# Kernel tuning notes

Hardware: AMD Instinct MI355X
Metric: run time of the kernel (lower is better)

## Reference

```python
import jax, jax.numpy as jnp
import numpy as np

TN_LAYERS = 2
GCN_LAYERS = 2

def _gru(x, h0, Wih, Whh, bih, bhh):
    # x: (B,T,I), h0: (B,H) -> (B,T,H); torch nn.GRU gate math (r,z,n ordering)
    def step(h, xt):
        gi = xt @ Wih.T + bih
        gh = h @ Whh.T + bhh
        ir, iz, inn = jnp.split(gi, 3, axis=-1)
        hr, hz, hn = jnp.split(gh, 3, axis=-1)
        r = jax.nn.sigmoid(ir + hr)
        z = jax.nn.sigmoid(iz + hz)
        n = jnp.tanh(inn + r * hn)
        h_new = (1.0 - z) * n + z * h
        return h_new, h_new
    _, hs = jax.lax.scan(step, h0, jnp.swapaxes(x, 0, 1))
    return jnp.swapaxes(hs, 0, 1)

def _forward(x, x_mark, sp_emb, sp_W1, sp_b1, sp_W2, sp_b2, t_emb, t_Wih, t_Whh, t_bih, t_bhh,
             gcn_W, gcn_b, fr_W1, fr_b1, fr_W2, fr_b2, tr_Wih, tr_Whh, tr_bih, tr_bhh, out_W, out_b):
    B, T, N = x.shape
    L = sp_b1.shape[0]
    elu = jax.nn.elu
    # --- SpatialEncoder: (B,N,T) ++ static embed -> Linear,ELU,Linear -> (B,N,L)
    xs = jnp.swapaxes(x, 1, 2)
    xs = jnp.concatenate([xs, jnp.broadcast_to(sp_emb, (B,) + sp_emb.shape)], axis=-1)
    Xs = elu(xs @ sp_W1 + sp_b1) @ sp_W2 + sp_b2
    # --- TemporalEncoder: concat(x, x_mark, static time embed) -> GRU -> (B,T,L)
    xt = jnp.concatenate([x, x_mark, jnp.broadcast_to(t_emb, (B,) + t_emb.shape)], axis=-1)
    Xt = _gru(xt, jnp.zeros((B, L), x.dtype), t_Wih, t_Whh, t_bih, t_bhh)
    X = jnp.concatenate([Xs, Xt], axis=1)  # (B, N+T, L)
    # --- TN modules: dynamic adjacency tanh(relu(X X^T)) + weighted message passing.
    # The torch code extracts per-batch sparse edge lists from batch_adj and does
    # gather-weight-scatter over them; zero-weight edges contribute nothing, so this
    # equals dense weighted aggregation A @ X per batch.
    for ti in range(TN_LAYERS):
        A = jnp.tanh(jax.nn.relu(jnp.einsum('bnf,bmf->bnm', X, X)))  # (B,N+T,N+T)
        for li in range(GCN_LAYERS):
            X = elu(jnp.einsum('bnm,bmd->bnd', A, X) @ gcn_W[ti, li] + gcn_b[ti, li])
    # --- Rebuild branches
    Xs2, Xt2 = X[:, :N, :], X[:, N:, :]
    rs = elu(Xs2 @ fr_W1 + fr_b1) @ fr_W2 + fr_b2  # feature_rebuild: (B,N,T)
    rt = _gru(Xt2, jnp.zeros((B, N), x.dtype), tr_Wih, tr_Whh, tr_bih, tr_bhh)  # time_rebuild: (B,T,N)
    combined = rs + jnp.swapaxes(rt, 1, 2)  # (B,N,T)
    return combined @ out_W + out_b  # (B, N, out_seq_len)

def setup_inputs():
    key = jax.random.key(0)
    B, T, N, Dt, L, E = 8, 96, 2000, 4, 32, 32
    ks = iter(jax.random.split(key, 32))
    nrm = lambda shape, s: jax.random.normal(next(ks), shape, jnp.float32) * s
    return {
        'x': nrm((B, T, N), 1.0),
        'x_mark': nrm((B, T, Dt), 1.0),
        'sp_emb': nrm((N, E), 0.1),
        'sp_W1': nrm((T + E, L), (T + E) ** -0.5), 'sp_b1': jnp.zeros((L,), jnp.float32),
        'sp_W2': nrm((L, L), L ** -0.5), 'sp_b2': jnp.zeros((L,), jnp.float32),
        't_emb': nrm((T, E), 0.1),
        't_Wih': nrm((3 * L, N + Dt + E), (N + Dt + E) ** -0.5),
        't_Whh': nrm((3 * L, L), L ** -0.5),
        't_bih': jnp.zeros((3 * L,), jnp.float32), 't_bhh': jnp.zeros((3 * L,), jnp.float32),
        'gcn_W': nrm((TN_LAYERS, GCN_LAYERS, L, L), 3e-3),  # small scale: dense aggregation sums ~N+T terms
        'gcn_b': jnp.zeros((TN_LAYERS, GCN_LAYERS, L), jnp.float32),
        'fr_W1': nrm((L, T), L ** -0.5), 'fr_b1': jnp.zeros((T,), jnp.float32),
        'fr_W2': nrm((T, T), T ** -0.5), 'fr_b2': jnp.zeros((T,), jnp.float32),
        'tr_Wih': nrm((3 * N, L), L ** -0.5), 'tr_Whh': nrm((3 * N, N), N ** -0.5),
        'tr_bih': jnp.zeros((3 * N,), jnp.float32), 'tr_bhh': jnp.zeros((3 * N,), jnp.float32),
        'out_W': nrm((T, 1), T ** -0.5), 'out_b': jnp.zeros((1,), jnp.float32),
    }

def reference(x, x_mark, sp_emb, sp_W1, sp_b1, sp_W2, sp_b2, t_emb, t_Wih, t_Whh, t_bih, t_bhh,
              gcn_W, gcn_b, fr_W1, fr_b1, fr_W2, fr_b2, tr_Wih, tr_Whh, tr_bih, tr_bhh, out_W, out_b):
    return _forward(x, x_mark, sp_emb, sp_W1, sp_b1, sp_W2, sp_b2, t_emb, t_Wih, t_Whh, t_bih, t_bhh,
                    gcn_W, gcn_b, fr_W1, fr_b1, fr_W2, fr_b2, tr_Wih, tr_Whh, tr_bih, tr_bhh, out_W, out_b)
```

## Files before the change

kernel.cpp:

```cpp
#include <hip/hip_runtime.h>

typedef _Float16 half8 __attribute__((ext_vector_type(8)));
typedef float f32x4 __attribute__((ext_vector_type(4)));

#define NBLK 125
#define BAR_INTS (NBLK * 32)

__global__ __launch_bounds__(256) void k_spatial(
    const float* __restrict__ x, const float* __restrict__ sp_emb,
    const float* __restrict__ W1, const float* __restrict__ b1,
    const float* __restrict__ W2, const float* __restrict__ b2,
    _Float16* __restrict__ X, int* __restrict__ bar, unsigned char* __restrict__ hA) {
  __shared__ float W1s[128 * 32];
  __shared__ float W2s[32 * 32];
  __shared__ float b1s[32], b2s[32];
  int tid = threadIdx.x;
  int gidx = blockIdx.x * 256 + tid;
  for (int i = gidx; i < BAR_INTS; i += 63 * 256) bar[i] = 0;
  for (int i = gidx; i < 4000; i += 63 * 256) ((unsigned int*)hA)[i] = 0u;
  for (int i = tid; i < 128 * 32; i += 256) W1s[i] = W1[i];
  for (int i = tid; i < 32 * 32; i += 256) W2s[i] = W2[i];
  if (tid < 32) { b1s[tid] = b1[tid]; b2s[tid] = b2[tid]; }
  __syncthreads();
  if (gidx >= 8 * 2000) return;
  int b = gidx / 2000, n = gidx % 2000;
  float h1[32];
#pragma unroll
  for (int l = 0; l < 32; l++) h1[l] = b1s[l];
  for (int k = 0; k < 96; k++) {
    float xv = x[((size_t)b * 96 + k) * 2000 + n];
#pragma unroll
    for (int l = 0; l < 32; l++) h1[l] = fmaf(xv, W1s[k * 32 + l], h1[l]);
  }
  for (int e4 = 0; e4 < 8; e4++) {
    float4 ev = *reinterpret_cast<const float4*>(&sp_emb[(size_t)n * 32 + e4 * 4]);
    float evs[4] = {ev.x, ev.y, ev.z, ev.w};
#pragma unroll
    for (int q = 0; q < 4; q++) {
      int e = e4 * 4 + q;
#pragma unroll
      for (int l = 0; l < 32; l++) h1[l] = fmaf(evs[q], W1s[(96 + e) * 32 + l], h1[l]);
    }
  }
  float out[32];
#pragma unroll
  for (int j = 0; j < 32; j++) out[j] = b2s[j];
  for (int l = 0; l < 32; l++) {
    float a = h1[l] > 0.0f ? h1[l] : (__expf(h1[l]) - 1.0f);
#pragma unroll
    for (int j = 0; j < 32; j++) out[j] = fmaf(a, W2s[l * 32 + j], out[j]);
  }
  _Float16* dst = X + ((size_t)b * 2096 + n) * 32;
#pragma unroll
  for (int j8 = 0; j8 < 4; j8++) {
    half8 v;
#pragma unroll
    for (int q = 0; q < 8; q++) v[q] = (_Float16)out[j8 * 8 + q];
    *reinterpret_cast<half8*>(dst + j8 * 8) = v;
  }
}

__global__ __launch_bounds__(256) void k_tgi(
    const float* __restrict__ x, const float* __restrict__ x_mark,
    const float* __restrict__ t_emb, const float* __restrict__ Wih,
    const float* __restrict__ bih, float* __restrict__ gi) {
  __shared__ float xs[8][2036];
  int tid = threadIdx.x;
  int row0 = blockIdx.x * 8;
  for (int rr = 0; rr < 8; rr++) {
    int row = row0 + rr;
    int b = row / 96, t = row % 96;
    for (int k = tid; k < 2036; k += 256) {
      float v;
      if (k < 2000) v = x[((size_t)b * 96 + t) * 2000 + k];
      else if (k < 2004) v = x_mark[((size_t)b * 96 + t) * 4 + (k - 2000)];
      else v = t_emb[(size_t)t * 32 + (k - 2004)];
      xs[rr][k] = v;
    }
  }
  __syncthreads();
  for (int oi = tid; oi < 8 * 96; oi += 256) {
    int rr = oi & 7, g = oi >> 3;
    const float* w = Wih + (size_t)g * 2036;
    float acc = bih[g];
    for (int k = 0; k < 2036; k += 4) {
      float4 wv = *reinterpret_cast<const float4*>(w + k);
      acc = fmaf(xs[rr][k + 0], wv.x, acc);
      acc = fmaf(xs[rr][k + 1], wv.y, acc);
      acc = fmaf(xs[rr][k + 2], wv.z, acc);
      acc = fmaf(xs[rr][k + 3], wv.w, acc);
    }
    gi[(size_t)(row0 + rr) * 96 + g] = acc;
  }
}

__global__ __launch_bounds__(768) void k_tgru(
    const float* __restrict__ gi, const float* __restrict__ Whh,
    const float* __restrict__ bhh, _Float16* __restrict__ X) {
  __shared__ float Whs[96][33];
  __shared__ float hs[8][33];
  __shared__ float ga[3][8][33];
  int tid = threadIdx.x;
  for (int i = tid; i < 96 * 32; i += 768) Whs[i >> 5][i & 31] = Whh[i];
  if (tid < 256) hs[tid >> 5][tid & 31] = 0.0f;
  int g = tid >> 8, j = (tid >> 3) & 31, b = tid & 7;
  int row = g * 32 + j;
  float bb0 = 0.f, bb1 = 0.f, bb2 = 0.f;
  if (tid < 256) {
    int jj = tid & 31;
    bb0 = bhh[jj]; bb1 = bhh[32 + jj]; bb2 = bhh[64 + jj];
  }
  __syncthreads();
  for (int t = 0; t < 96; t++) {
    float acc = 0.0f;
#pragma unroll
    for (int k = 0; k < 32; k++) acc = fmaf(hs[b][k], Whs[row][k], acc);
    ga[g][b][j] = acc;
    __syncthreads();
    if (tid < 256) {
      int bb = tid >> 5, jj = tid & 31;
      const float* gp = gi + ((size_t)bb * 96 + t) * 96;
      float gr = ga[0][bb][jj] + bb0;
      float gz = ga[1][bb][jj] + bb1;
      float gn = ga[2][bb][jj] + bb2;
      float r = 1.0f / (1.0f + __expf(-(gp[jj] + gr)));
      float z = 1.0f / (1.0f + __expf(-(gp[32 + jj] + gz)));
      float n = tanhf(gp[64 + jj] + r * gn);
      float hn = (1.0f - z) * n + z * hs[bb][jj];
      hs[bb][jj] = hn;
      X[((size_t)bb * 2096 + 2000 + t) * 32 + jj] = (_Float16)hn;
    }
    __syncthreads();
  }
}

__global__ __launch_bounds__(256) void k_gnn(
    const _Float16* __restrict__ Xa, const _Float16* __restrict__ Xin,
    _Float16* __restrict__ Xout, const float* __restrict__ W,
    const float* __restrict__ bias) {
  __shared__ _Float16 XaR[32][40];
  __shared__ _Float16 Xm[2][64][40];
  __shared__ _Float16 Xq[2][64][40];
  __shared__ _Float16 At[32][72];
  __shared__ float Pm[32][36];
  __shared__ float Ws[32][36];
  __shared__ float bs[32];
  int tid = threadIdx.x;
  int l = tid & 63, w = tid >> 6;
  int b = blockIdx.y;
  int r0 = blockIdx.x * 32;
  const _Float16* Xab = Xa + (size_t)b * 2096 * 32;
  const _Float16* Xib = Xin + (size_t)b * 2096 * 32;
  half8 hz = {(_Float16)0, (_Float16)0, (_Float16)0, (_Float16)0,
              (_Float16)0, (_Float16)0, (_Float16)0, (_Float16)0};

  for (int i = tid; i < 1024; i += 256) Ws[i >> 5][i & 31] = W[i];
  if (tid < 32) bs[tid] = bias[tid];
  if (tid < 128) {
    int r = tid >> 2, k = (tid & 3) * 8;
    half8 v = (r0 + r < 2096)
                  ? *reinterpret_cast<const half8*>(Xab + (size_t)(r0 + r) * 32 + k)
                  : hz;
    *reinterpret_cast<half8*>(&XaR[r][k]) = v;
  }
  int sr = tid >> 2, sk = (tid & 3) * 8;
  {
    *reinterpret_cast<half8*>(&Xm[0][sr][sk]) =
        *reinterpret_cast<const half8*>(Xab + (size_t)sr * 32 + sk);
    *reinterpret_cast<half8*>(&Xq[0][sr][sk]) =
        *reinterpret_cast<const half8*>(Xib + (size_t)sr * 32 + sk);
  }
  __syncthreads();

  int lr = l & 15, lk = (l >> 4) * 8, lq = (l >> 4) * 4;
  int smt = w >> 1, snt2 = w & 1;
  int pmt = w >> 1, pnt = w & 1;
  half8 afrag = *reinterpret_cast<const half8*>(&XaR[smt * 16 + lr][lk]);
  f32x4 pacc = {0.f, 0.f, 0.f, 0.f};

  for (int tt = 0; tt < 33; tt++) {
    int cur = tt & 1, nb = cur ^ 1;
    half8 vm = hz, vq = hz;
    bool hv = (tt + 1 < 33);
    if (hv) {
      int gm = (tt + 1) * 64 + sr;
      if (gm < 2096) {
        vm = *reinterpret_cast<const half8*>(Xab + (size_t)gm * 32 + sk);
        vq = *reinterpret_cast<const half8*>(Xib + (size_t)gm * 32 + sk);
      }
    }
#pragma unroll
    for (int n16 = 0; n16 < 2; n16++) {
      int c0 = snt2 * 32 + n16 * 16;
      half8 bfrag = *reinterpret_cast<const half8*>(&Xm[cur][c0 + lr][lk]);
      f32x4 s4 = __builtin_amdgcn_mfma_f32_16x16x32_f16(
          afrag, bfrag, (f32x4){0.f, 0.f, 0.f, 0.f}, 0, 0, 0);
#pragma unroll
      for (int j = 0; j < 4; j++) {
        float e = __expf(-2.0f * fmaxf(s4[j], 0.0f));
        At[smt * 16 + lq + j][c0 + lr] = (_Float16)((1.0f - e) / (1.0f + e));
      }
    }
    __syncthreads();
#pragma unroll
    for (int kc = 0; kc < 2; kc++) {
      half8 af = *reinterpret_cast<const half8*>(&At[pmt * 16 + lr][kc * 32 + lk]);
      half8 bf;
      int kb = kc * 32 + lk;
      int nn = pnt * 16 + lr;
#pragma unroll
      for (int e = 0; e < 8; e++) bf[e] = Xq[cur][kb + e][nn];
      pacc = __builtin_amdgcn_mfma_f32_16x16x32_f16(af, bf, pacc, 0, 0, 0);
    }
    if (hv) {
      *reinterpret_cast<half8*>(&Xm[nb][sr][sk]) = vm;
      *reinterpret_cast<half8*>(&Xq[nb][sr][sk]) = vq;
    }
    __syncthreads();
  }

#pragma unroll
  for (int j = 0; j < 4; j++) Pm[pmt * 16 + lq + j][pnt * 16 + lr] = pacc[j];
  __syncthreads();
  int r = tid & 31, fgr = tid >> 5;
  int f0 = fgr * 4;
  float o[4];
#pragma unroll
  for (int j = 0; j < 4; j++) o[j] = bs[f0 + j];
#pragma unroll
  for (int k = 0; k < 32; k++) {
    float mv = Pm[r][k];
    float4 wv = *reinterpret_cast<const float4*>(&Ws[k][f0]);
    o[0] = fmaf(mv, wv.x, o[0]);
    o[1] = fmaf(mv, wv.y, o[1]);
    o[2] = fmaf(mv, wv.z, o[2]);
    o[3] = fmaf(mv, wv.w, o[3]);
  }
  int grr = r0 + r;
  if (grr < 2096) {
    _Float16* dst = Xout + ((size_t)b * 2096 + grr) * 32 + f0;
#pragma unroll
    for (int j = 0; j < 4; j++) {
      float v = o[j];
      dst[j] = (_Float16)(v > 0.0f ? v : (__expf(v) - 1.0f));
    }
  }
}

__global__ __launch_bounds__(1024) void k_trgru(
    const _Float16* __restrict__ X, const float* __restrict__ wih,
    const float* __restrict__ bih, float* __restrict__ gi,
    const float* __restrict__ whh, const float* __restrict__ bhh,
    unsigned char* __restrict__ hA, unsigned char* __restrict__ hB,
    float* __restrict__ rt, int* __restrict__ seq,
    const float* __restrict__ frW1, const float* __restrict__ frb1,
    const float* __restrict__ frW2, const float* __restrict__ frb2,
    float* __restrict__ rs) {
  __shared__ __align__(16) unsigned char SM[139264];
  int tid = threadIdx.x;
  int blk = blockIdx.x;

  if (blk >= NBLK) {
    float* W1s = (float*)(SM);
    float* W2s = (float*)(SM + 12288);
    float* b1s = (float*)(SM + 50688);
    float* b2s = (float*)(SM + 51072);
    float* Xt  = (float*)(SM + 51456);
    float* Hl  = (float*)(SM + 55680);
    for (int i = tid; i < 32 * 96; i += 1024) W1s[i] = frW1[i];
    for (int i = tid; i < 96 * 96; i += 1024) W2s[(i / 96) * 100 + (i % 96)] = frW2[i];
    if (tid < 96) { b1s[tid] = frb1[tid]; b2s[tid] = frb2[tid]; }
    __syncthreads();
    for (int ti = blk - NBLK; ti < 504; ti += NBLK) {
      int b = ti / 63, n0 = (ti % 63) * 32;
      {
        int r = tid >> 5, k = tid & 31;
        Xt[r * 33 + k] =
            (n0 + r < 2000) ? (float)X[((size_t)b * 2096 + n0 + r) * 32 + k] : 0.0f;
      }
      __syncthreads();
#pragma unroll
      for (int q = 0; q < 3; q++) {
        int idx = q * 1024 + tid;
        int r = idx / 96, c = idx % 96;
        float a = b1s[c];
#pragma unroll 8
        for (int k = 0; k < 32; k++) a = fmaf(Xt[r * 33 + k], W1s[k * 96 + c], a);
        Hl[r * 100 + c] = a > 0.0f ? a : (__expf(a) - 1.0f);
      }
      __syncthreads();
#pragma unroll
      for (int q = 0; q < 3; q++) {
        int idx = q * 1024 + tid;
        int r = idx / 96, c = idx % 96;
        float o = b2s[c];
#pragma unroll 8
        for (int k = 0; k < 96; k++) o = fmaf(Hl[r * 100 + k], W2s[k * 100 + c], o);
        if (n0 + r < 2000) rs[((size_t)b * 2000 + n0 + r) * 96 + c] = o;
      }
      __syncthreads();
    }
    return;
  }

  unsigned char* wf = SM;
  unsigned char* hf = SM + 98304;
  float* pt = (float*)(SM + 114688);
  int l = tid & 63, w = tid >> 6;

  for (int i = tid; i < 12288; i += 1024) ((unsigned long long*)wf)[i] = 0ull;
  for (int i = tid; i < 2048; i += 1024) ((unsigned long long*)hf)[i] = 0ull;

  if (tid < 768) {
    int t = tid >> 3, b = tid & 7;
    float xr[32];
    const _Float16* xp = X + ((size_t)b * 2096 + 2000 + t) * 32;
#pragma unroll
    for (int k = 0; k < 32; k++) xr[k] = (float)xp[k];
    float* gp = gi + ((size_t)b * 96 + t) * 6000;
    for (int g = 0; g < 3; g++) {
#pragma unroll
      for (int j = 0; j < 16; j++) {
        int row = g * 2000 + blk * 16 + j;
        const float* wr = wih + (size_t)row * 32;
        float a = bih[row];
#pragma unroll 8
        for (int k = 0; k < 32; k++) a = fmaf(xr[k], wr[k], a);
        gp[row] = a;
      }
    }
  }
  __syncthreads();

  for (int i = tid; i < 3 * 64 * 64; i += 1024) {
    int g = i >> 12;
    int c = (i >> 6) & 63;
    int l2 = i & 63;
    int j = l2 & 15;
    int k0 = c * 32 + ((l2 >> 4) << 3);
    if (k0 <= 1992) {
      const float* src = whh + ((size_t)(g * 2000 + blk * 16 + j)) * 2000 + k0;
      float4 v0 = *reinterpret_cast<const float4*>(src);
      float4 v1 = *reinterpret_cast<const float4*>(src + 4);
      unsigned int lo = __builtin_amdgcn_cvt_pk_fp8_f32(v0.x, v0.y, 0, false);
      lo = __builtin_amdgcn_cvt_pk_fp8_f32(v0.z, v0.w, lo, true);
      unsigned int hi = __builtin_amdgcn_cvt_pk_fp8_f32(v1.x, v1.y, 0, false);
      hi = __builtin_amdgcn_cvt_pk_fp8_f32(v1.z, v1.w, hi, true);
      unsigned long long q = ((unsigned long long)hi << 32) | (unsigned long long)lo;
      *reinterpret_cast<unsigned long long*>(wf + (size_t)g * 32768 + c * 512 + l2 * 8) = q;
    }
  }

  int cj = tid >> 3, cb = tid & 7;
  int jg = blk * 16 + cj;
  float hold = 0.0f, bR = 0.f, bZ = 0.f, bN = 0.f;
  if (tid < 128) {
    bR = bhh[jg]; bZ = bhh[2000 + jg]; bN = bhh[4000 + jg];
  }
  int bslot = ((l >> 4) * 8 + (l & 7)) * 8;
  __syncthreads();

  for (int t = 0; t < 96; t++) {
    const unsigned char* hc = (t & 1) ? hB : hA;
    unsigned char* hn = (t & 1) ? hA : hB;
    float gir = 0.f, giz = 0.f, gin = 0.f;
    if (tid < 128) {
      const float* gp = gi + ((size_t)cb * 96 + t) * 6000;
      gir = gp[jg]; giz = gp[2000 + jg]; gin = gp[4000 + jg];
    }
    for (int i = tid; i < 2048; i += 1024) {
      int c = i >> 5, s = i & 31;
      int b = s & 7;
      int k0 = c * 32 + ((s >> 3) << 3);
      if (k0 < 2000) {
        unsigned long long v =
            *reinterpret_cast<const unsigned long long*>(hc + b * 2000 + k0);
        *reinterpret_cast<unsigned long long*>(hf + c * 256 + s * 8) = v;
      }
    }
    __syncthreads();
    f32x4 a0 = {0.f, 0.f, 0.f, 0.f}, a1 = {0.f, 0.f, 0.f, 0.f}, a2 = {0.f, 0.f, 0.f, 0.f};
#pragma unroll
    for (int i = 0; i < 4; i++) {
      int c = w * 4 + i;
      long long bv = *reinterpret_cast<const long long*>(hf + c * 256 + bslot);
      long long w0 = *reinterpret_cast<const long long*>(wf + 0 * 32768 + c * 512 + l * 8);
      long long w1 = *reinterpret_cast<const long long*>(wf + 1 * 32768 + c * 512 + l * 8);
      long long w2 = *reinterpret_cast<const long long*>(wf + 2 * 32768 + c * 512 + l * 8);
      a0 = __builtin_amdgcn_mfma_f32_16x16x32_fp8_fp8(w0, bv, a0, 0, 0, 0);
      a1 = __builtin_amdgcn_mfma_f32_16x16x32_fp8_fp8(w1, bv, a1, 0, 0, 0);
      a2 = __builtin_amdgcn_mfma_f32_16x16x32_fp8_fp8(w2, bv, a2, 0, 0, 0);
    }
    {
      int bcol = l & 15;
      if (bcol < 8) {
        int lb = l >> 4;
        *reinterpret_cast<f32x4*>(pt + w * 384 + 0 * 128 + lb * 32 + bcol * 4) = a0;
        *reinterpret_cast<f32x4*>(pt + w * 384 + 1 * 128 + lb * 32 + bcol * 4) = a1;
        *reinterpret_cast<f32x4*>(pt + w * 384 + 2 * 128 + lb * 32 + bcol * 4) = a2;
      }
    }
    __syncthreads();
    if (tid < 128) {
      float s[3];
#pragma unroll
      for (int g = 0; g < 3; g++) {
        int base = g * 128 + (cj >> 2) * 32 + cb * 4 + (cj & 3);
        float acc = 0.f;
#pragma unroll
        for (int w2 = 0; w2 < 16; w2++) acc += pt[w2 * 384 + base];
        s[g] = acc;
      }
      float r_ = 1.0f / (1.0f + __expf(-(gir + s[0] + bR)));
      float z_ = 1.0f / (1.0f + __expf(-(giz + s[1] + bZ)));
      float n_ = tanhf(gin + r_ * (s[2] + bN));
      hold = (1.0f - z_) * n_ + z_ * hold;
      {
        unsigned int p = __builtin_amdgcn_cvt_pk_fp8_f32(hold, 0.0f, 0, false);
        __hip_atomic_store(hn + cb * 2000 + jg, (unsigned char)(p & 0xFF),
                           __ATOMIC_RELAXED, __HIP_MEMORY_SCOPE_AGENT);
      }
      rt[((size_t)cb * 96 + t) * 2000 + jg] = hold;
    }
    __syncthreads();
    if (tid == 0) {
      __hip_atomic_store(&seq[blk * 32], t + 1, __ATOMIC_RELAXED,
                         __HIP_MEMORY_SCOPE_AGENT);
    }
    if ((tid >> 6) == 2) {
      int lane = tid & 63;
      const int* s1 = &seq[lane * 32];
      const int* s2 = &seq[((lane + 64) < NBLK ? (lane + 64) : lane) * 32];
      while (true) {
        int v1 = __hip_atomic_load(s1, __ATOMIC_RELAXED, __HIP_MEMORY_SCOPE_AGENT);
        int v2 = __hip_atomic_load(s2, __ATOMIC_RELAXED, __HIP_MEMORY_SCOPE_AGENT);
        if (__all(v1 > t && v2 > t)) break;
        __builtin_amdgcn_s_sleep(1);
      }
      if (lane == 0) {
        (void)__hip_atomic_load(s1, __ATOMIC_ACQUIRE, __HIP_MEMORY_SCOPE_AGENT);
      }
    }
    __syncthreads();
  }
}

__global__ __launch_bounds__(256) void k_final(
    const float* __restrict__ rs, const float* __restrict__ rt,
    const float* __restrict__ outW, const float* __restrict__ outb,
    float* __restrict__ out) {
  __shared__ float w[96];
  __shared__ float ob;
  int tid = threadIdx.x;
  if (tid < 96) w[tid] = outW[tid];
  if (tid == 0) ob = outb[0];
  __syncthreads();
  int gidx = blockIdx.x * 256 + tid;
  if (gidx >= 16000) return;
  int b = gidx / 2000, n = gidx % 2000;
  const float* rsp = rs + (size_t)gidx * 96;
  float acc = ob;
  for (int t4 = 0; t4 < 24; t4++) {
    float4 rv = *reinterpret_cast<const float4*>(rsp + t4 * 4);
    int t = t4 * 4;
    acc = fmaf(rv.x + rt[((size_t)b * 96 + t + 0) * 2000 + n], w[t + 0], acc);
    acc = fmaf(rv.y + rt[((size_t)b * 96 + t + 1) * 2000 + n], w[t + 1], acc);
    acc = fmaf(rv.z + rt[((size_t)b * 96 + t + 2) * 2000 + n], w[t + 2], acc);
    acc = fmaf(rv.w + rt[((size_t)b * 96 + t + 3) * 2000 + n], w[t + 3], acc);
  }
  out[gidx] = acc;
}

extern "C" void kernel_launch(void* const* d_in, const int* in_sizes, int n_in,
                              void* d_out, int out_size, void* d_ws, size_t ws_size,
                              hipStream_t stream) {
  const float* x      = (const float*)d_in[0];
  const float* x_mark = (const float*)d_in[1];
  const float* sp_emb = (const float*)d_in[2];
  const float* sp_W1  = (const float*)d_in[3];
  const float* sp_b1  = (const float*)d_in[4];
  const float* sp_W2  = (const float*)d_in[5];
  const float* sp_b2  = (const float*)d_in[6];
  const float* t_emb  = (const float*)d_in[7];
  const float* t_Wih  = (const float*)d_in[8];
  const float* t_Whh  = (const float*)d_in[9];
  const float* t_bih  = (const float*)d_in[10];
  const float* t_bhh  = (const float*)d_in[11];
  const float* gcn_W  = (const float*)d_in[12];
  const float* gcn_b  = (const float*)d_in[13];
  const float* fr_W1  = (const float*)d_in[14];
  const float* fr_b1  = (const float*)d_in[15];
  const float* fr_W2  = (const float*)d_in[16];
  const float* fr_b2  = (const float*)d_in[17];
  const float* tr_Wih = (const float*)d_in[18];
  const float* tr_Whh = (const float*)d_in[19];
  const float* tr_bih = (const float*)d_in[20];
  const float* tr_bhh = (const float*)d_in[21];
  const float* out_W  = (const float*)d_in[22];
  const float* out_b  = (const float*)d_in[23];
  (void)in_sizes; (void)n_in; (void)out_size; (void)ws_size;

  float* ws = (float*)d_ws;
  float* X0   = ws;
  float* X1   = X0 + 536576;
  float* X2   = X1 + 536576;
  float* tgi  = X2 + 536576;
  float* trgi = tgi + 73728;
  float* hsl  = trgi + 4608000;
  float* rt   = hsl + 16000;
  float* rs   = rt + 1536000;
  float* barf = rs + 1536000;

  _Float16* X0h = (_Float16*)X0;
  _Float16* X1h = (_Float16*)X1;
  _Float16* X2h = (_Float16*)X2;
  unsigned char* hA = (unsigned char*)hsl;
  unsigned char* hB = hA + 16000;
  int* seq = (int*)barf;

  k_spatial<<<63, 256, 0, stream>>>(x, sp_emb, sp_W1, sp_b1, sp_W2, sp_b2, X0h, seq, hA);
  k_tgi<<<96, 256, 0, stream>>>(x, x_mark, t_emb, t_Wih, t_bih, tgi);
  k_tgru<<<1, 768, 0, stream>>>(tgi, t_Whh, t_bhh, X0h);

  dim3 gg(66, 8);
  k_gnn<<<gg, 256, 0, stream>>>(X0h, X0h, X1h, gcn_W + 0 * 1024, gcn_b + 0 * 32);
  k_gnn<<<gg, 256, 0, stream>>>(X0h, X1h, X2h, gcn_W + 1 * 1024, gcn_b + 1 * 32);
  k_gnn<<<gg, 256, 0, stream>>>(X2h, X2h, X0h, gcn_W + 2 * 1024, gcn_b + 2 * 32);
  k_gnn<<<gg, 256, 0, stream>>>(X2h, X0h, X1h, gcn_W + 3 * 1024, gcn_b + 3 * 32);

  {
    const _Float16* a0 = X1h;
    const float* a1 = tr_Wih;
    const float* a2 = tr_bih;
    float* a3 = trgi;
    const float* a4 = tr_Whh;
    const float* a5 = tr_bhh;
    unsigned char* a6 = hA;
    unsigned char* a7 = hB;
    float* a8 = rt;
    int* a9 = seq;
    const float* a10 = fr_W1;
    const float* a11 = fr_b1;
    const float* a12 = fr_W2;
    const float* a13 = fr_b2;
    float* a14 = rs;
    void* cargs[] = {&a0, &a1, &a2, &a3, &a4, &a5, &a6, &a7,
                     &a8, &a9, &a10, &a11, &a12, &a13, &a14};
    hipLaunchCooperativeKernel((const void*)k_trgru, dim3(250), dim3(1024), cargs, 0, stream);
  }

  k_final<<<63, 256, 0, stream>>>(rs, rt, out_W, out_b, (float*)d_out);
}
```

Measured before the change: 1.001 ms.

## Merge prologue kernels, fuse final projection into cooperative GRU, transpose GNN operand

```diff
diff --git a/kernel.cpp b/kernel.cpp
--- a/kernel.cpp
+++ b/kernel.cpp
@@ -4,93 +4,96 @@
 typedef float f32x4 __attribute__((ext_vector_type(4)));
 
 #define NBLK 125
-#define BAR_INTS (NBLK * 32)
-
-__global__ __launch_bounds__(256) void k_spatial(
-    const float* __restrict__ x, const float* __restrict__ sp_emb,
-    const float* __restrict__ W1, const float* __restrict__ b1,
-    const float* __restrict__ W2, const float* __restrict__ b2,
-    _Float16* __restrict__ X, int* __restrict__ bar, unsigned char* __restrict__ hA) {
-  __shared__ float W1s[128 * 32];
-  __shared__ float W2s[32 * 32];
-  __shared__ float b1s[32], b2s[32];
+#define TOTBLK 250
+#define BAR_INTS (TOTBLK * 32)
+
+__global__ __launch_bounds__(256) void k_pre(
+    const float* __restrict__ x, const float* __restrict__ x_mark,
+    const float* __restrict__ sp_emb,
+    const float* __restrict__ spW1, const float* __restrict__ spb1,
+    const float* __restrict__ spW2, const float* __restrict__ spb2,
+    const float* __restrict__ t_emb, const float* __restrict__ tWih,
+    const float* __restrict__ tbih,
+    _Float16* __restrict__ X, float* __restrict__ gi,
+    int* __restrict__ seq, unsigned char* __restrict__ hA) {
+  __shared__ __align__(16) unsigned char PSM[65152];
   int tid = threadIdx.x;
-  int gidx = blockIdx.x * 256 + tid;
-  for (int i = gidx; i < BAR_INTS; i += 63 * 256) bar[i] = 0;
-  for (int i = gidx; i < 4000; i += 63 * 256) ((unsigned int*)hA)[i] = 0u;
-  for (int i = tid; i < 128 * 32; i += 256) W1s[i] = W1[i];
-  for (int i = tid; i < 32 * 32; i += 256) W2s[i] = W2[i];
-  if (tid < 32) { b1s[tid] = b1[tid]; b2s[tid] = b2[tid]; }
-  __syncthreads();
-  if (gidx >= 8 * 2000) return;
-  int b = gidx / 2000, n = gidx % 2000;
-  float h1[32];
-#pragma unroll
-  for (int l = 0; l < 32; l++) h1[l] = b1s[l];
-  for (int k = 0; k < 96; k++) {
-    float xv = x[((size_t)b * 96 + k) * 2000 + n];
-#pragma unroll
-    for (int l = 0; l < 32; l++) h1[l] = fmaf(xv, W1s[k * 32 + l], h1[l]);
-  }
-  for (int e4 = 0; e4 < 8; e4++) {
-    float4 ev = *reinterpret_cast<const float4*>(&sp_emb[(size_t)n * 32 + e4 * 4]);
-    float evs[4] = {ev.x, ev.y, ev.z, ev.w};
-#pragma unroll
-    for (int q = 0; q < 4; q++) {
-      int e = e4 * 4 + q;
-#pragma unroll
-      for (int l = 0; l < 32; l++) h1[l] = fmaf(evs[q], W1s[(96 + e) * 32 + l], h1[l]);
-    }
-  }
-  float out[32];
-#pragma unroll
-  for (int j = 0; j < 32; j++) out[j] = b2s[j];
-  for (int l = 0; l < 32; l++) {
-    float a = h1[l] > 0.0f ? h1[l] : (__expf(h1[l]) - 1.0f);
-#pragma unroll
-    for (int j = 0; j < 32; j++) out[j] = fmaf(a, W2s[l * 32 + j], out[j]);
-  }
-  _Float16* dst = X + ((size_t)b * 2096 + n) * 32;
-#pragma unroll
-  for (int j8 = 0; j8 < 4; j8++) {
-    half8 v;
-#pragma unroll
-    for (int q = 0; q < 8; q++) v[q] = (_Float16)out[j8 * 8 + q];
-    *reinterpret_cast<half8*>(dst + j8 * 8) = v;
-  }
-}
-
-__global__ __launch_bounds__(256) void k_tgi(
-    const float* __restrict__ x, const float* __restrict__ x_mark,
-    const float* __restrict__ t_emb, const float* __restrict__ Wih,
-    const float* __restrict__ bih, float* __restrict__ gi) {
-  __shared__ float xs[8][2036];
-  int tid = threadIdx.x;
-  int row0 = blockIdx.x * 8;
-  for (int rr = 0; rr < 8; rr++) {
-    int row = row0 + rr;
-    int b = row / 96, t = row % 96;
-    for (int k = tid; k < 2036; k += 256) {
-      float v;
-      if (k < 2000) v = x[((size_t)b * 96 + t) * 2000 + k];
-      else if (k < 2004) v = x_mark[((size_t)b * 96 + t) * 4 + (k - 2000)];
-      else v = t_emb[(size_t)t * 32 + (k - 2004)];
-      xs[rr][k] = v;
-    }
-  }
-  __syncthreads();
-  for (int oi = tid; oi < 8 * 96; oi += 256) {
-    int rr = oi & 7, g = oi >> 3;
-    const float* w = Wih + (size_t)g * 2036;
-    float acc = bih[g];
-    for (int k = 0; k < 2036; k += 4) {
-      float4 wv = *reinterpret_cast<const float4*>(w + k);
-      acc = fmaf(xs[rr][k + 0], wv.x, acc);
-      acc = fmaf(xs[rr][k + 1], wv.y, acc);
-      acc = fmaf(xs[rr][k + 2], wv.z, acc);
-      acc = fmaf(xs[rr][k + 3], wv.w, acc);
-    }
-    gi[(size_t)(row0 + rr) * 96 + g] = acc;
+  if (blockIdx.x < 63) {
+    float* W1s = (float*)PSM;
+    float* W2s = (float*)(PSM + 16384);
+    float* b1s = (float*)(PSM + 20480);
+    float* b2s = (float*)(PSM + 20608);
+    int gidx = blockIdx.x * 256 + tid;
+    for (int i = gidx; i < BAR_INTS; i += 63 * 256) seq[i] = 0;
+    for (int i = gidx; i < 4000; i += 63 * 256) ((unsigned int*)hA)[i] = 0u;
+    for (int i = tid; i < 128 * 32; i += 256) W1s[i] = spW1[i];
+    for (int i = tid; i < 32 * 32; i += 256) W2s[i] = spW2[i];
+    if (tid < 32) { b1s[tid] = spb1[tid]; b2s[tid] = spb2[tid]; }
+    __syncthreads();
+    if (gidx >= 8 * 2000) return;
+    int b = gidx / 2000, n = gidx % 2000;
+    float h1[32];
+#pragma unroll
+    for (int l = 0; l < 32; l++) h1[l] = b1s[l];
+    for (int k = 0; k < 96; k++) {
+      float xv = x[((size_t)b * 96 + k) * 2000 + n];
+#pragma unroll
+      for (int l = 0; l < 32; l++) h1[l] = fmaf(xv, W1s[k * 32 + l], h1[l]);
+    }
+    for (int e4 = 0; e4 < 8; e4++) {
+      float4 ev = *reinterpret_cast<const float4*>(&sp_emb[(size_t)n * 32 + e4 * 4]);
+      float evs[4] = {ev.x, ev.y, ev.z, ev.w};
+#pragma unroll
+      for (int q = 0; q < 4; q++) {
+        int e = e4 * 4 + q;
+#pragma unroll
+        for (int l = 0; l < 32; l++) h1[l] = fmaf(evs[q], W1s[(96 + e) * 32 + l], h1[l]);
+      }
+    }
+    float out[32];
+#pragma unroll
+    for (int j = 0; j < 32; j++) out[j] = b2s[j];
+    for (int l = 0; l < 32; l++) {
+      float a = h1[l] > 0.0f ? h1[l] : (__expf(h1[l]) - 1.0f);
+#pragma unroll
+      for (int j = 0; j < 32; j++) out[j] = fmaf(a, W2s[l * 32 + j], out[j]);
+    }
+    _Float16* dst = X + ((size_t)b * 2096 + n) * 32;
+#pragma unroll
+    for (int j8 = 0; j8 < 4; j8++) {
+      half8 v;
+#pragma unroll
+      for (int q = 0; q < 8; q++) v[q] = (_Float16)out[j8 * 8 + q];
+      *reinterpret_cast<half8*>(dst + j8 * 8) = v;
+    }
+  } else {
+    float (*xs)[2036] = (float(*)[2036])PSM;
+    int row0 = (blockIdx.x - 63) * 8;
+    for (int rr = 0; rr < 8; rr++) {
+      int row = row0 + rr;
+      int b = row / 96, t = row % 96;
+      for (int k = tid; k < 2036; k += 256) {
+        float v;
+        if (k < 2000) v = x[((size_t)b * 96 + t) * 2000 + k];
+        else if (k < 2004) v = x_mark[((size_t)b * 96 + t) * 4 + (k - 2000)];
+        else v = t_emb[(size_t)t * 32 + (k - 2004)];
+        xs[rr][k] = v;
+      }
+    }
+    __syncthreads();
+    for (int oi = tid; oi < 8 * 96; oi += 256) {
+      int rr = oi & 7, g = oi >> 3;
+      const float* w = tWih + (size_t)g * 2036;
+      float acc = tbih[g];
+      for (int k = 0; k < 2036; k += 4) {
+        float4 wv = *reinterpret_cast<const float4*>(w + k);
+        acc = fmaf(xs[rr][k + 0], wv.x, acc);
+        acc = fmaf(xs[rr][k + 1], wv.y, acc);
+        acc = fmaf(xs[rr][k + 2], wv.z, acc);
+        acc = fmaf(xs[rr][k + 3], wv.w, acc);
+      }
+      gi[(size_t)(row0 + rr) * 96 + g] = acc;
+    }
   }
 }
 
@@ -140,7 +143,7 @@
     const float* __restrict__ bias) {
   __shared__ _Float16 XaR[32][40];
   __shared__ _Float16 Xm[2][64][40];
-  __shared__ _Float16 Xq[2][64][40];
+  __shared__ _Float16 XqT[2][32][72];
   __shared__ _Float16 At[32][72];
   __shared__ float Pm[32][36];
   __shared__ float Ws[32][36];
@@ -167,8 +170,9 @@
   {
     *reinterpret_cast<half8*>(&Xm[0][sr][sk]) =
         *reinterpret_cast<const half8*>(Xab + (size_t)sr * 32 + sk);
-    *reinterpret_cast<half8*>(&Xq[0][sr][sk]) =
-        *reinterpret_cast<const half8*>(Xib + (size_t)sr * 32 + sk);
+    half8 vq = *reinterpret_cast<const half8*>(Xib + (size_t)sr * 32 + sk);
+#pragma unroll
+    for (int e = 0; e < 8; e++) XqT[0][sk + e][sr] = vq[e];
   }
   __syncthreads();
 
@@ -202,19 +206,19 @@
       }
     }
     __syncthreads();
-#pragma unroll
-    for (int kc = 0; kc < 2; kc++) {
-      half8 af = *reinterpret_cast<const half8*>(&At[pmt * 16 + lr][kc * 32 + lk]);
-      half8 bf;
-      int kb = kc * 32 + lk;
+    {
       int nn = pnt * 16 + lr;
 #pragma unroll
-      for (int e = 0; e < 8; e++) bf[e] = Xq[cur][kb + e][nn];
-      pacc = __builtin_amdgcn_mfma_f32_16x16x32_f16(af, bf, pacc, 0, 0, 0);
+      for (int kc = 0; kc < 2; kc++) {
+        half8 af = *reinterpret_cast<const half8*>(&At[pmt * 16 + lr][kc * 32 + lk]);
+        half8 bf = *reinterpret_cast<const half8*>(&XqT[cur][nn][kc * 32 + lk]);
+        pacc = __builtin_amdgcn_mfma_f32_16x16x32_f16(af, bf, pacc, 0, 0, 0);
+      }
     }
     if (hv) {
       *reinterpret_cast<half8*>(&Xm[nb][sr][sk]) = vm;
-      *reinterpret_cast<half8*>(&Xq[nb][sr][sk]) = vq;
+#pragma unroll
+      for (int e = 0; e < 8; e++) XqT[nb][sk + e][sr] = vq[e];
     }
     __syncthreads();
   }
@@ -255,8 +259,9 @@
     float* __restrict__ rt, int* __restrict__ seq,
     const float* __restrict__ frW1, const float* __restrict__ frb1,
     const float* __restrict__ frW2, const float* __restrict__ frb2,
-    float* __restrict__ rs) {
-  __shared__ __align__(16) unsigned char SM[139264];
+    float* __restrict__ rs, const float* __restrict__ outW,
+    const float* __restrict__ outb, float* __restrict__ out) {
+  __shared__ __align__(16) unsigned char SM[122880];
   int tid = threadIdx.x;
   int blk = blockIdx.x;
 
@@ -296,179 +301,190 @@
         float o = b2s[c];
 #pragma unroll 8
         for (int k = 0; k < 96; k++) o = fmaf(Hl[r * 100 + k], W2s[k * 100 + c], o);
-        if (n0 + r < 2000) rs[((size_t)b * 2000 + n0 + r) * 96 + c] = o;
+        if (n0 + r < 2000) {
+          __hip_atomic_store(&rs[((size_t)b * 2000 + n0 + r) * 96 + c], o,
+                             __ATOMIC_RELAXED, __HIP_MEMORY_SCOPE_AGENT);
+        }
       }
       __syncthreads();
     }
-    return;
-  }
-
-  unsigned char* wf = SM;
-  unsigned char* hf = SM + 98304;
-  float* pt = (float*)(SM + 114688);
-  int l = tid & 63, w = tid >> 6;
-
-  for (int i = tid; i < 12288; i += 1024) ((unsigned long long*)wf)[i] = 0ull;
-  for (int i = tid; i < 2048; i += 1024) ((unsigned long long*)hf)[i] = 0ull;
-
-  if (tid < 768) {
-    int t = tid >> 3, b = tid & 7;
-    float xr[32];
-    const _Float16* xp = X + ((size_t)b * 2096 + 2000 + t) * 32;
-#pragma unroll
-    for (int k = 0; k < 32; k++) xr[k] = (float)xp[k];
-    float* gp = gi + ((size_t)b * 96 + t) * 6000;
-    for (int g = 0; g < 3; g++) {
-#pragma unroll
-      for (int j = 0; j < 16; j++) {
-        int row = g * 2000 + blk * 16 + j;
-        const float* wr = wih + (size_t)row * 32;
-        float a = bih[row];
+    if (tid == 0) {
+      __hip_atomic_store(&seq[blk * 32], 96, __ATOMIC_RELAXED,
+                         __HIP_MEMORY_SCOPE_AGENT);
+    }
+  } else {
+    unsigned char* wf = SM;
+    float* pt = (float*)(SM + 98304);
+    int l = tid & 63, w = tid >> 6;
+
+    for (int i = tid; i < 12288; i += 1024) ((unsigned long long*)wf)[i] = 0ull;
+
+    if (tid < 768) {
+      int t = tid >> 3, b = tid & 7;
+      float xr[32];
+      const _Float16* xp = X + ((size_t)b * 2096 + 2000 + t) * 32;
+#pragma unroll
+      for (int k = 0; k < 32; k++) xr[k] = (float)xp[k];
+      float* gp = gi + ((size_t)b * 96 + t) * 6000;
+      for (int g = 0; g < 3; g++) {
+#pragma unroll
+        for (int j = 0; j < 16; j++) {
+          int row = g * 2000 + blk * 16 + j;
+          const float* wr = wih + (size_t)row * 32;
+          float a = bih[row];
 #pragma unroll 8
-        for (int k = 0; k < 32; k++) a = fmaf(xr[k], wr[k], a);
-        gp[row] = a;
-      }
-    }
-  }
-  __syncthreads();
-
-  for (int i = tid; i < 3 * 64 * 64; i += 1024) {
-    int g = i >> 12;
-    int c = (i >> 6) & 63;
-    int l2 = i & 63;
-    int j = l2 & 15;
-    int k0 = c * 32 + ((l2 >> 4) << 3);
-    if (k0 <= 1992) {
-      const float* src = whh + ((size_t)(g * 2000 + blk * 16 + j)) * 2000 + k0;
-      float4 v0 = *reinterpret_cast<const float4*>(src);
-      float4 v1 = *reinterpret_cast<const float4*>(src + 4);
-      unsigned int lo = __builtin_amdgcn_cvt_pk_fp8_f32(v0.x, v0.y, 0, false);
-      lo = __builtin_amdgcn_cvt_pk_fp8_f32(v0.z, v0.w, lo, true);
-      unsigned int hi = __builtin_amdgcn_cvt_pk_fp8_f32(v1.x, v1.y, 0, false);
-      hi = __builtin_amdgcn_cvt_pk_fp8_f32(v1.z, v1.w, hi, true);
-      unsigned long long q = ((unsigned long long)hi << 32) | (unsigned long long)lo;
-      *reinterpret_cast<unsigned long long*>(wf + (size_t)g * 32768 + c * 512 + l2 * 8) = q;
-    }
-  }
-
-  int cj = tid >> 3, cb = tid & 7;
-  int jg = blk * 16 + cj;
-  float hold = 0.0f, bR = 0.f, bZ = 0.f, bN = 0.f;
-  if (tid < 128) {
-    bR = bhh[jg]; bZ = bhh[2000 + jg]; bN = bhh[4000 + jg];
-  }
-  int bslot = ((l >> 4) * 8 + (l & 7)) * 8;
-  __syncthreads();
-
-  for (int t = 0; t < 96; t++) {
-    const unsigned char* hc = (t & 1) ? hB : hA;
-    unsigned char* hn = (t & 1) ? hA : hB;
-    float gir = 0.f, giz = 0.f, gin = 0.f;
+          for (int k = 0; k < 32; k++) a = fmaf(xr[k], wr[k], a);
+          gp[row] = a;
+        }
+      }
+    }
+
+    for (int i = tid; i < 3 * 64 * 64; i += 1024) {
+      int g = i >> 12;
+      int c = (i >> 6) & 63;
+      int l2 = i & 63;
+      int j = l2 & 15;
+      int k0 = c * 32 + ((l2 >> 4) << 3);
+      if (k0 <= 1992) {
+        const float* src = whh + ((size_t)(g * 2000 + blk * 16 + j)) * 2000 + k0;
+        float4 v0 = *reinterpret_cast<const float4*>(src);
+        float4 v1 = *reinterpret_cast<const float4*>(src + 4);
+        unsigned int lo = __builtin_amdgcn_cvt_pk_fp8_f32(v0.x, v0.y, 0, false);
+        lo = __builtin_amdgcn_cvt_pk_fp8_f32(v0.z, v0.w, lo, true);
+        unsigned int hi = __builtin_amdgcn_cvt_pk_fp8_f32(v1.x, v1.y, 0, false);
+        hi = __builtin_amdgcn_cvt_pk_fp8_f32(v1.z, v1.w, hi, true);
+        unsigned long long q = ((unsigned long long)hi << 32) | (unsigned long long)lo;
+        *reinterpret_cast<unsigned long long*>(wf + (size_t)g * 32768 + c * 512 + l2 * 8) = q;
+      }
+    }
+
+    int cj = tid >> 3, cb = tid & 7;
+    int jg = blk * 16 + cj;
+    float hold = 0.0f, bR = 0.f, bZ = 0.f, bN = 0.f;
     if (tid < 128) {
-      const float* gp = gi + ((size_t)cb * 96 + t) * 6000;
-      gir = gp[jg]; giz = gp[2000 + jg]; gin = gp[4000 + jg];
-    }
-    for (int i = tid; i < 2048; i += 1024) {
-      int c = i >> 5, s = i & 31;
-      int b = s & 7;
-      int k0 = c * 32 + ((s >> 3) << 3);
-      if (k0 < 2000) {
-        unsigned long long v =
-            *reinterpret_cast<const unsigned long long*>(hc + b * 2000 + k0);
-        *reinterpret_cast<unsigned long long*>(hf + c * 256 + s * 8) = v;
-      }
-    }
-    __syncthreads();
-    f32x4 a0 = {0.f, 0.f, 0.f, 0.f}, a1 = {0.f, 0.f, 0.f, 0.f}, a2 = {0.f, 0.f, 0.f, 0.f};
-#pragma unroll
-    for (int i = 0; i < 4; i++) {
-      int c = w * 4 + i;
-      long long bv = *reinterpret_cast<const long long*>(hf + c * 256 + bslot);
-      long long w0 = *reinterpret_cast<const long long*>(wf + 0 * 32768 + c * 512 + l * 8);
-      long long w1 = *reinterpret_cast<const long long*>(wf + 1 * 32768 + c * 512 + l * 8);
-      long long w2 = *reinterpret_cast<const long long*>(wf + 2 * 32768 + c * 512 + l * 8);
-      a0 = __builtin_amdgcn_mfma_f32_16x16x32_fp8_fp8(w0, bv, a0, 0, 0, 0);
-      a1 = __builtin_amdgcn_mfma_f32_16x16x32_fp8_fp8(w1, bv, a1, 0, 0, 0);
-      a2 = __builtin_amdgcn_mfma_f32_16x16x32_fp8_fp8(w2, bv, a2, 0, 0, 0);
-    }
-    {
-      int bcol = l & 15;
-      if (bcol < 8) {
-        int lb = l >> 4;
-        *reinterpret_cast<f32x4*>(pt + w * 384 + 0 * 128 + lb * 32 + bcol * 4) = a0;
-        *reinterpret_cast<f32x4*>(pt + w * 384 + 1 * 128 + lb * 32 + bcol * 4) = a1;
-        *reinterpret_cast<f32x4*>(pt + w * 384 + 2 * 128 + lb * 32 + bcol * 4) = a2;
-      }
-    }
-    __syncthreads();
-    if (tid < 128) {
-      float s[3];
-#pragma unroll
-      for (int g = 0; g < 3; g++) {
-        int base = g * 128 + (cj >> 2) * 32 + cb * 4 + (cj & 3);
-        float acc = 0.f;
-#pragma unroll
-        for (int w2 = 0; w2 < 16; w2++) acc += pt[w2 * 384 + base];
-        s[g] = acc;
-      }
-      float r_ = 1.0f / (1.0f + __expf(-(gir + s[0] + bR)));
-      float z_ = 1.0f / (1.0f + __expf(-(giz + s[1] + bZ)));
-      float n_ = tanhf(gin + r_ * (s[2] + bN));
-      hold = (1.0f - z_) * n_ + z_ * hold;
+      bR = bhh[jg]; bZ = bhh[2000 + jg]; bN = bhh[4000 + jg];
+    }
+    int bb = l & 7, kblk = (l >> 4) * 8;
+    __syncthreads();
+
+    for (int t = 0; t < 96; t++) {
+      const unsigned char* hc = (t & 1) ? hB : hA;
+      unsigned char* hn = (t & 1) ? hA : hB;
+      float gir = 0.f, giz = 0.f, gin = 0.f;
+      if (tid < 128) {
+        const float* gp = gi + ((size_t)cb * 96 + t) * 6000;
+        gir = gp[jg]; giz = gp[2000 + jg]; gin = gp[4000 + jg];
+      }
+      f32x4 a0 = {0.f, 0.f, 0.f, 0.f}, a1 = {0.f, 0.f, 0.f, 0.f}, a2 = {0.f, 0.f, 0.f, 0.f};
+#pragma unroll
+      for (int i = 0; i < 4; i++) {
+        int c = w * 4 + i;
+        int k0 = c * 32 + kblk;
+        long long bv = 0;
+        if (k0 <= 1992)
+          bv = *reinterpret_cast<const long long*>(hc + bb * 2000 + k0);
+        long long w0 = *reinterpret_cast<const long long*>(wf + 0 * 32768 + c * 512 + l * 8);
+        long long w1 = *reinterpret_cast<const long long*>(wf + 1 * 32768 + c * 512 + l * 8);
+        long long w2 = *reinterpret_cast<const long long*>(wf + 2 * 32768 + c * 512 + l * 8);
+        a0 = __builtin_amdgcn_mfma_f32_16x16x32_fp8_fp8(w0, bv, a0, 0, 0, 0);
+        a1 = __builtin_amdgcn_mfma_f32_16x16x32_fp8_fp8(w1, bv, a1, 0, 0, 0);
+        a2 = __builtin_amdgcn_mfma_f32_16x16x32_fp8_fp8(w2, bv, a2, 0, 0, 0);
+      }
       {
-        unsigned int p = __builtin_amdgcn_cvt_pk_fp8_f32(hold, 0.0f, 0, false);
-        __hip_atomic_store(hn + cb * 2000 + jg, (unsigned char)(p & 0xFF),
+        int bcol = l & 15;
+        if (bcol < 8) {
+          int lb = l >> 4;
+          *reinterpret_cast<f32x4*>(pt + w * 384 + 0 * 128 + lb * 32 + bcol * 4) = a0;
+          *reinterpret_cast<f32x4*>(pt + w * 384 + 1 * 128 + lb * 32 + bcol * 4) = a1;
+          *reinterpret_cast<f32x4*>(pt + w * 384 + 2 * 128 + lb * 32 + bcol * 4) = a2;
+        }
+      }
+      __syncthreads();
+      if (tid < 128) {
+        float s[3];
+#pragma unroll
+        for (int g = 0; g < 3; g++) {
+          int base = g * 128 + (cj >> 2) * 32 + cb * 4 + (cj & 3);
+          float acc = 0.f;
+#pragma unroll
+          for (int w2 = 0; w2 < 16; w2++) acc += pt[w2 * 384 + base];
+          s[g] = acc;
+        }
+        float r_ = 1.0f / (1.0f + __expf(-(gir + s[0] + bR)));
+        float z_ = 1.0f / (1.0f + __expf(-(giz + s[1] + bZ)));
+        float n_ = tanhf(gin + r_ * (s[2] + bN));
+        hold = (1.0f - z_) * n_ + z_ * hold;
+        {
+          unsigned int p = __builtin_amdgcn_cvt_pk_fp8_f32(hold, 0.0f, 0, false);
+          __hip_atomic_store(hn + cb * 2000 + jg, (unsigned char)(p & 0xFF),
+                             __ATOMIC_RELAXED, __HIP_MEMORY_SCOPE_AGENT);
+        }
+        __hip_atomic_store(&rt[((size_t)cb * 96 + t) * 2000 + jg], hold,
                            __ATOMIC_RELAXED, __HIP_MEMORY_SCOPE_AGENT);
       }
-      rt[((size_t)cb * 96 + t) * 2000 + jg] = hold;
-    }
-    __syncthreads();
-    if (tid == 0) {
-      __hip_atomic_store(&seq[blk * 32], t + 1, __ATOMIC_RELAXED,
-                         __HIP_MEMORY_SCOPE_AGENT);
-    }
-    if ((tid >> 6) == 2) {
-      int lane = tid & 63;
-      const int* s1 = &seq[lane * 32];
-      const int* s2 = &seq[((lane + 64) < NBLK ? (lane + 64) : lane) * 32];
+      __syncthreads();
+      if (tid == 0) {
+        __hip_atomic_store(&seq[blk * 32], t + 1, __ATOMIC_RELAXED,
+                           __HIP_MEMORY_SCOPE_AGENT);
+      }
+      if ((tid >> 6) == 2) {
+        int lane = tid & 63;
+        const int* s1 = &seq[lane * 32];
+        const int* s2 = &seq[((lane + 64) < NBLK ? (lane + 64) : lane) * 32];
+        while (true) {
+          int v1 = __hip_atomic_load(s1, __ATOMIC_RELAXED, __HIP_MEMORY_SCOPE_AGENT);
+          int v2 = __hip_atomic_load(s2, __ATOMIC_RELAXED, __HIP_MEMORY_SCOPE_AGENT);
+          if (__all(v1 > t && v2 > t)) break;
+          __builtin_amdgcn_s_sleep(1);
+        }
+        if (lane == 0) {
+          (void)__hip_atomic_load(s1, __ATOMIC_ACQUIRE, __HIP_MEMORY_SCOPE_AGENT);
+        }
+      }
+      __syncthreads();
+    }
+  }
+
+  {
+    float* wsm = (float*)SM;
+    __syncthreads();
+    if (tid >= 128 && tid < 224) wsm[tid - 128] = outW[tid - 128];
+    if (tid == 224) wsm[96] = outb[0];
+    if (tid < 64) {
+      const int* p0 = &seq[tid * 32];
+      const int* p1 = &seq[(tid + 64) * 32];
+      const int* p2 = &seq[(tid + 128) * 32];
+      int i3 = tid + 192; if (i3 >= TOTBLK) i3 = tid;
+      const int* p3 = &seq[i3 * 32];
       while (true) {
-        int v1 = __hip_atomic_load(s1, __ATOMIC_RELAXED, __HIP_MEMORY_SCOPE_AGENT);
-        int v2 = __hip_atomic_load(s2, __ATOMIC_RELAXED, __HIP_MEMORY_SCOPE_AGENT);
-        if (__all(v1 > t && v2 > t)) break;
-        __builtin_amdgcn_s_sleep(1);
-      }
-      if (lane == 0) {
-        (void)__hip_atomic_load(s1, __ATOMIC_ACQUIRE, __HIP_MEMORY_SCOPE_AGENT);
-      }
-    }
-    __syncthreads();
-  }
-}
-
-__global__ __launch_bounds__(256) void k_final(
-    const float* __restrict__ rs, const float* __restrict__ rt,
-    const float* __restrict__ outW, const float* __restrict__ outb,
-    float* __restrict__ out) {
-  __shared__ float w[96];
-  __shared__ float ob;
-  int tid = threadIdx.x;
-  if (tid < 96) w[tid] = outW[tid];
-  if (tid == 0) ob = outb[0];
-  __syncthreads();
-  int gidx = blockIdx.x * 256 + tid;
-  if (gidx >= 16000) return;
-  int b = gidx / 2000, n = gidx % 2000;
-  const float* rsp = rs + (size_t)gidx * 96;
-  float acc = ob;
-  for (int t4 = 0; t4 < 24; t4++) {
-    float4 rv = *reinterpret_cast<const float4*>(rsp + t4 * 4);
-    int t = t4 * 4;
-    acc = fmaf(rv.x + rt[((size_t)b * 96 + t + 0) * 2000 + n], w[t + 0], acc);
-    acc = fmaf(rv.y + rt[((size_t)b * 96 + t + 1) * 2000 + n], w[t + 1], acc);
-    acc = fmaf(rv.z + rt[((size_t)b * 96 + t + 2) * 2000 + n], w[t + 2], acc);
-    acc = fmaf(rv.w + rt[((size_t)b * 96 + t + 3) * 2000 + n], w[t + 3], acc);
-  }
-  out[gidx] = acc;
+        int v0 = __hip_atomic_load(p0, __ATOMIC_RELAXED, __HIP_MEMORY_SCOPE_AGENT);
+        int v1 = __hip_atomic_load(p1, __ATOMIC_RELAXED, __HIP_MEMORY_SCOPE_AGENT);
+        int v2 = __hip_atomic_load(p2, __ATOMIC_RELAXED, __HIP_MEMORY_SCOPE_AGENT);
+        int v3 = __hip_atomic_load(p3, __ATOMIC_RELAXED, __HIP_MEMORY_SCOPE_AGENT);
+        if (__all(v0 >= 96 && v1 >= 96 && v2 >= 96 && v3 >= 96)) break;
+        __builtin_amdgcn_s_sleep(2);
+      }
+      if (tid == 0) {
+        (void)__hip_atomic_load(p0, __ATOMIC_ACQUIRE, __HIP_MEMORY_SCOPE_AGENT);
+      }
+    }
+    __syncthreads();
+    if (tid < 64) {
+      int idx = blk * 64 + tid;
+      int b = idx / 2000, n = idx % 2000;
+      const float* rsp = rs + (size_t)idx * 96;
+      float acc = wsm[96];
+      for (int t4 = 0; t4 < 24; t4++) {
+        float4 rv = *reinterpret_cast<const float4*>(rsp + t4 * 4);
+        int t = t4 * 4;
+        acc = fmaf(rv.x + rt[((size_t)b * 96 + t + 0) * 2000 + n], wsm[t + 0], acc);
+        acc = fmaf(rv.y + rt[((size_t)b * 96 + t + 1) * 2000 + n], wsm[t + 1], acc);
+        acc = fmaf(rv.z + rt[((size_t)b * 96 + t + 2) * 2000 + n], wsm[t + 2], acc);
+        acc = fmaf(rv.w + rt[((size_t)b * 96 + t + 3) * 2000 + n], wsm[t + 3], acc);
+      }
+      out[idx] = acc;
+    }
+  }
 }
 
 extern "C" void kernel_launch(void* const* d_in, const int* in_sizes, int n_in,
@@ -518,8 +534,8 @@
   unsigned char* hB = hA + 16000;
   int* seq = (int*)barf;
 
-  k_spatial<<<63, 256, 0, stream>>>(x, sp_emb, sp_W1, sp_b1, sp_W2, sp_b2, X0h, seq, hA);
-  k_tgi<<<96, 256, 0, stream>>>(x, x_mark, t_emb, t_Wih, t_bih, tgi);
+  k_pre<<<159, 256, 0, stream>>>(x, x_mark, sp_emb, sp_W1, sp_b1, sp_W2, sp_b2,
+                                 t_emb, t_Wih, t_bih, X0h, tgi, seq, hA);
   k_tgru<<<1, 768, 0, stream>>>(tgi, t_Whh, t_bhh, X0h);
 
   dim3 gg(66, 8);
@@ -544,10 +560,11 @@
     const float* a12 = fr_W2;
     const float* a13 = fr_b2;
     float* a14 = rs;
-    void* cargs[] = {&a0, &a1, &a2, &a3, &a4, &a5, &a6, &a7,
-                     &a8, &a9, &a10, &a11, &a12, &a13, &a14};
-    hipLaunchCooperativeKernel((const void*)k_trgru, dim3(250), dim3(1024), cargs, 0, stream);
-  }
-
-  k_final<<<63, 256, 0, stream>>>(rs, rt, out_W, out_b, (float*)d_out);
+    const float* a15 = out_W;
+    const float* a16 = out_b;
+    float* a17 = (float*)d_out;
+    void* cargs[] = {&a0, &a1, &a2, &a3, &a4, &a5, &a6, &a7, &a8, &a9,
+                     &a10, &a11, &a12, &a13, &a14, &a15, &a16, &a17};
+    hipLaunchCooperativeKernel((const void*)k_trgru, dim3(TOTBLK), dim3(1024), cargs, 0, stream);
+  }
 }
```

Result: faster. 932.1 us (-6.9%).
